# Optimization experiments

Measured on AMD Instinct MI355X. Metric: run time of the kernel, lower is better.

The kernel has to match this reference:

```python
import jax, jax.numpy as jnp
import numpy as np

N_NODES = 100000
N_EDGES = 1600000
NFEAT = 256
NHID = 64
NHEADS = 8
NCLASS = 97
ALPHA = 0.2  # leaky relu slope
EPS = 1e-16  # guard against isolated rows (pyGAT divides by e_rowsum directly)


def _sp_gat_layer(x, Wk, ak, src, dst, n_nodes, alpha, concat):
    """One SpGraphAttentionLayer (eval mode, dropout off).
    x: [N, f_in], Wk: [f_in, f_out], ak: [2*f_out].
    edge e_ij = exp(-leakyrelu(a . [h_i || h_j])), out[i] = sum_j e_ij h_j / sum_j e_ij.
    """
    h = x @ Wk                          # [N, f_out]
    f_out = Wk.shape[1]
    s_src = h @ ak[:f_out]              # [N] = a1 . h_i
    s_dst = h @ ak[f_out:]              # [N] = a2 . h_j
    e = jnp.exp(-jax.nn.leaky_relu(s_src[src] + s_dst[dst], negative_slope=alpha))  # [E]
    rowsum = jax.ops.segment_sum(e, src, num_segments=n_nodes)                       # [N]
    num = jax.ops.segment_sum(e[:, None] * h[dst], src, num_segments=n_nodes)        # [N, f_out]
    h_prime = num / (rowsum[:, None] + EPS)
    return jax.nn.elu(h_prime) if concat else h_prime


def setup_inputs() -> dict:
    key = jax.random.key(0)
    ks = jax.random.split(key, 6)
    gain = 1.414  # xavier gain used by pyGAT
    features = jax.random.normal(ks[0], (N_NODES, NFEAT), dtype=jnp.float32)
    edge_index = jax.random.randint(ks[1], (2, N_EDGES), 0, N_NODES, dtype=jnp.int64)
    W = jax.random.normal(ks[2], (NHEADS, NFEAT, NHID), dtype=jnp.float32) * (gain * np.sqrt(2.0 / (NFEAT + NHID)))
    a = jax.random.normal(ks[3], (NHEADS, 2 * NHID), dtype=jnp.float32) * (gain * np.sqrt(2.0 / (1 + 2 * NHID)))
    W_out = jax.random.normal(ks[4], (NHEADS * NHID, NCLASS), dtype=jnp.float32) * (gain * np.sqrt(2.0 / (NHEADS * NHID + NCLASS)))
    a_out = jax.random.normal(ks[5], (2 * NCLASS,), dtype=jnp.float32) * (gain * np.sqrt(2.0 / (1 + 2 * NCLASS)))
    return {"features": features, "W": W, "a": a, "W_out": W_out, "a_out": a_out, "edge_index": edge_index}


def reference(features, W, a, W_out, a_out, edge_index):
    src, dst = edge_index[0], edge_index[1]
    n = features.shape[0]
    # multi-head hidden layer, concat heads (loop over small fixed head count to bound memory)
    heads = [
        _sp_gat_layer(features, W[k], a[k], src, dst, n, ALPHA, concat=True)
        for k in range(W.shape[0])
    ]
    x = jnp.concatenate(heads, axis=1)  # [N, nheads*nhid]
    # output attention layer (concat=False), then elu + log_softmax as in SpGAT.forward
    x = _sp_gat_layer(x, W_out, a_out, src, dst, n, ALPHA, concat=False)
    return jax.nn.log_softmax(jax.nn.elu(x), axis=1)
```

## Files before the change

kernel.cpp:

```cpp
#include <hip/hip_runtime.h>
#include <hip/hip_bf16.h>
#include <stdint.h>

typedef __attribute__((ext_vector_type(8))) short short8;
typedef __attribute__((ext_vector_type(4))) float floatx4;
typedef uint32_t u32;

#define N_NODES 100000
#define N_EDGES 1600000
#define ALPHA_SLOPE 0.2f
#define EPS_F 1e-16f

static __device__ __forceinline__ float bf2f(ushort h) {
    u32 u = ((u32)h) << 16;
    return __builtin_bit_cast(float, u);
}
static __device__ __forceinline__ ushort f2bf(float f) {
    u32 u = __builtin_bit_cast(u32, f);
    u32 r = (u + 0x7fffu + ((u >> 16) & 1u)) >> 16;
    return (ushort)r;
}

__global__ __launch_bounds__(256) void conv_feat(
    const float* __restrict__ in, ushort* __restrict__ out, int n4)
{
    int i = blockIdx.x * 256 + threadIdx.x;
    if (i < n4) {
        float4 v = ((const float4*)in)[i];
        ushort4 o;
        o.x = f2bf(v.x); o.y = f2bf(v.y); o.z = f2bf(v.z); o.w = f2bf(v.w);
        ((ushort4*)out)[i] = o;
    }
}

__global__ __launch_bounds__(256) void pretranspose(
    const float* __restrict__ W, const float* __restrict__ Wout,
    const float* __restrict__ a, const float* __restrict__ aout,
    ushort* __restrict__ Bp1, ushort* __restrict__ Bp2,
    float* __restrict__ acol1, float* __restrict__ acol2)
{
    int idx = blockIdx.x * 256 + threadIdx.x;
    if (idx < 256 * 512) {
        int k = idx >> 9, n = idx & 511;
        int head = n >> 6, c = n & 63;
        Bp1[((size_t)(k >> 3) * 512 + n) * 8 + (k & 7)] = f2bf(W[head * 16384 + k * 64 + c]);
    }
    if (idx < 512 * 128) {
        int k = idx >> 7, n = idx & 127;
        ushort v = (n < 97) ? f2bf(Wout[k * 97 + n]) : (ushort)0;
        Bp2[((size_t)(k >> 3) * 128 + n) * 8 + (k & 7)] = v;
    }
    if (idx < 512) {
        int head = idx >> 6, c = idx & 63;
        acol1[idx * 2]     = a[head * 128 + c];
        acol1[idx * 2 + 1] = a[head * 128 + 64 + c];
    }
    if (idx < 128) {
        acol2[idx * 2]     = (idx < 97) ? aout[idx] : 0.f;
        acol2[idx * 2 + 1] = (idx < 97) ? aout[97 + idx] : 0.f;
    }
}

__global__ __launch_bounds__(256) void gemm_mfma(
    const ushort* __restrict__ A, const ushort* __restrict__ Bp,
    ushort* __restrict__ C, const float* __restrict__ acol,
    float* __restrict__ spair, int M, int K, int NP)
{
    __shared__ __align__(16) ushort Ald[4 * 128 * 8];
    const int tid = threadIdx.x;
    const int lane = tid & 63;
    const int wave = tid >> 6;
    const int wr = wave >> 1, wc = wave & 1;
    const int row0 = blockIdx.x * 128;
    const int col0 = blockIdx.y * 128;
    const int quad = lane >> 4;
    const int l16 = lane & 15;

    floatx4 acc[4][4] = {};

    for (int k0 = 0; k0 < K; k0 += 32) {
        __syncthreads();
#pragma unroll
        for (int i = 0; i < 2; ++i) {
            int q = i * 256 + tid;
            int r = q >> 2, kq = q & 3;
            int row = row0 + r;
            if (row >= M) row = M - 1;
            const uint4* src = (const uint4*)(A + (size_t)row * K + k0 + kq * 8);
            *(uint4*)(&Ald[((kq * 128 + r) * 8)]) = *src;
        }
        __syncthreads();

        short8 bfrag[4];
        int kqg = (k0 >> 3) + quad;
#pragma unroll
        for (int nt = 0; nt < 4; ++nt) {
            int col = col0 + wc * 64 + nt * 16 + l16;
            bfrag[nt] = *(const short8*)(Bp + ((size_t)kqg * NP + col) * 8);
        }
#pragma unroll
        for (int mt = 0; mt < 4; ++mt) {
            int r = wr * 64 + mt * 16 + l16;
            short8 afrag = *(const short8*)(&Ald[(quad * 128 + r) * 8]);
#pragma unroll
            for (int nt = 0; nt < 4; ++nt) {
                acc[mt][nt] = __builtin_amdgcn_mfma_f32_16x16x32_bf16(afrag, bfrag[nt], acc[mt][nt], 0, 0, 0);
            }
        }
    }

#pragma unroll
    for (int mt = 0; mt < 4; ++mt) {
#pragma unroll
        for (int rr = 0; rr < 4; ++rr) {
            int row = row0 + wr * 64 + mt * 16 + quad * 4 + rr;
            if (row < M) {
#pragma unroll
                for (int nt = 0; nt < 4; ++nt) {
                    int col = col0 + wc * 64 + nt * 16 + l16;
                    C[(size_t)row * NP + col] = f2bf(acc[mt][nt][rr]);
                }
            }
        }
    }

    float av1[4], av2[4];
#pragma unroll
    for (int nt = 0; nt < 4; ++nt) {
        int col = col0 + wc * 64 + nt * 16 + l16;
        av1[nt] = acol[col * 2];
        av2[nt] = acol[col * 2 + 1];
    }
    int g = (col0 + wc * 64) >> 6;
    int ng = NP >> 6;
#pragma unroll
    for (int mt = 0; mt < 4; ++mt) {
#pragma unroll
        for (int rr = 0; rr < 4; ++rr) {
            float p1 = 0.f, p2 = 0.f;
#pragma unroll
            for (int nt = 0; nt < 4; ++nt) {
                p1 = fmaf(acc[mt][nt][rr], av1[nt], p1);
                p2 = fmaf(acc[mt][nt][rr], av2[nt], p2);
            }
#pragma unroll
            for (int o = 1; o < 16; o <<= 1) {
                p1 += __shfl_xor(p1, o);
                p2 += __shfl_xor(p2, o);
            }
            int row = row0 + wr * 64 + mt * 16 + quad * 4 + rr;
            if (l16 == 0 && row < M) {
                atomicAdd(&spair[((size_t)row * ng + g) * 2], p1);
                atomicAdd(&spair[((size_t)row * ng + g) * 2 + 1], p2);
            }
        }
    }
}

__global__ __launch_bounds__(256) void hist(const int* __restrict__ ei, int* __restrict__ cnt, int E) {
    int e = blockIdx.x * 256 + threadIdx.x;
    if (e < E) atomicAdd(&cnt[ei[e]], 1);
}

__global__ __launch_bounds__(256) void scan_partial(const int* __restrict__ cnt, int* __restrict__ bsum, int N) {
    int idx = blockIdx.x * 256 + threadIdx.x;
    int v = (idx < N) ? cnt[idx] : 0;
#pragma unroll
    for (int o = 32; o; o >>= 1) v += __shfl_xor(v, o);
    __shared__ int ws[4];
    if ((threadIdx.x & 63) == 0) ws[threadIdx.x >> 6] = v;
    __syncthreads();
    if (threadIdx.x == 0) bsum[blockIdx.x] = ws[0] + ws[1] + ws[2] + ws[3];
}

__global__ __launch_bounds__(512) void scan_block(int* __restrict__ bsum, int nb) {
    __shared__ int s[512];
    int t = threadIdx.x;
    int v = (t < nb) ? bsum[t] : 0;
    s[t] = v;
    __syncthreads();
    for (int o = 1; o < 512; o <<= 1) {
        int u = (t >= o) ? s[t - o] : 0;
        __syncthreads();
        s[t] += u;
        __syncthreads();
    }
    if (t < nb) bsum[t] = s[t] - v;
}

__global__ __launch_bounds__(256) void scan_final(
    const int* __restrict__ cnt, const int* __restrict__ bsum,
    int* __restrict__ row_ptr, int N, int E)
{
    int b = blockIdx.x, t = threadIdx.x;
    int idx = b * 256 + t;
    int v = (idx < N) ? cnt[idx] : 0;
    __shared__ int s[256];
    s[t] = v;
    __syncthreads();
    for (int o = 1; o < 256; o <<= 1) {
        int u = (t >= o) ? s[t - o] : 0;
        __syncthreads();
        s[t] += u;
        __syncthreads();
    }
    if (idx < N) row_ptr[idx] = bsum[b] + s[t] - v;
    if (idx == 0) row_ptr[N] = E;
}

__global__ __launch_bounds__(256) void fill_csr(
    const int* __restrict__ ei, const int* __restrict__ row_ptr,
    int* __restrict__ cur, int* __restrict__ col_idx, int* __restrict__ srow,
    const float* __restrict__ spair1, float* __restrict__ ew1, int E)
{
    int e = blockIdx.x * 256 + threadIdx.x;
    if (e >= E) return;
    int s = ei[e];
    int d = ei[E + e];
    int p = atomicAdd(&cur[s], 1);
    int slot = row_ptr[s] + p;
    col_idx[slot] = d;
    srow[slot] = s;
    const float4* qs = (const float4*)(spair1 + (size_t)s * 16);
    const float4* qd = (const float4*)(spair1 + (size_t)d * 16);
    float ev[8];
#pragma unroll
    for (int h4 = 0; h4 < 4; ++h4) {
        float4 vs = qs[h4];
        float4 vd = qd[h4];
        float v0 = vs.x + vd.y;
        float v1 = vs.z + vd.w;
        float l0 = v0 > 0.f ? v0 : ALPHA_SLOPE * v0;
        float l1 = v1 > 0.f ? v1 : ALPHA_SLOPE * v1;
        ev[2 * h4] = __expf(-l0);
        ev[2 * h4 + 1] = __expf(-l1);
    }
    float4* dst = (float4*)(ew1 + (size_t)slot * 8);
    dst[0] = make_float4(ev[0], ev[1], ev[2], ev[3]);
    dst[1] = make_float4(ev[4], ev[5], ev[6], ev[7]);
}

__global__ __launch_bounds__(256) void ea1(
    const int* __restrict__ row_ptr, const int* __restrict__ col_idx,
    const ushort* __restrict__ h_all, const float* __restrict__ ew1,
    ushort* __restrict__ x1)
{
    int w = blockIdx.x * 4 + (threadIdx.x >> 6);
    int l = threadIdx.x & 63;
    int hl = l >> 3;
    int start = row_ptr[w], end = row_ptr[w + 1];
    float acc[8] = {};
    float re = 0.f;
    int j = start;
    for (; j + 4 <= end; j += 4) {
        int d0 = col_idx[j], d1 = col_idx[j + 1], d2 = col_idx[j + 2], d3 = col_idx[j + 3];
        float e0 = ew1[(size_t)j * 8 + hl];
        float e1 = ew1[(size_t)(j + 1) * 8 + hl];
        float e2 = ew1[(size_t)(j + 2) * 8 + hl];
        float e3 = ew1[(size_t)(j + 3) * 8 + hl];
        short8 v0 = *(const short8*)(h_all + (size_t)d0 * 512 + l * 8);
        short8 v1 = *(const short8*)(h_all + (size_t)d1 * 512 + l * 8);
        short8 v2 = *(const short8*)(h_all + (size_t)d2 * 512 + l * 8);
        short8 v3 = *(const short8*)(h_all + (size_t)d3 * 512 + l * 8);
        re += (e0 + e1) + (e2 + e3);
#pragma unroll
        for (int q = 0; q < 8; ++q) {
            float t0 = fmaf(e0, bf2f((ushort)v0[q]), e1 * bf2f((ushort)v1[q]));
            float t1 = fmaf(e2, bf2f((ushort)v2[q]), e3 * bf2f((ushort)v3[q]));
            acc[q] += t0 + t1;
        }
    }
    for (; j < end; ++j) {
        int d = col_idx[j];
        float e = ew1[(size_t)j * 8 + hl];
        short8 hv = *(const short8*)(h_all + (size_t)d * 512 + l * 8);
        re += e;
#pragma unroll
        for (int q = 0; q < 8; ++q)
            acc[q] = fmaf(e, bf2f((ushort)hv[q]), acc[q]);
    }
    float inv = 1.f / (re + EPS_F);
    short8 o;
#pragma unroll
    for (int q = 0; q < 8; ++q) {
        float p = acc[q] * inv;
        p = p > 0.f ? p : expm1f(p);
        o[q] = (short)f2bf(p);
    }
    *(short8*)(x1 + (size_t)w * 512 + l * 8) = o;
}

__global__ __launch_bounds__(256) void ew2k(
    const int* __restrict__ srow, const int* __restrict__ col_idx,
    const float* __restrict__ spair2, float* __restrict__ ew2, int E)
{
    int j = blockIdx.x * 256 + threadIdx.x;
    if (j < E) {
        float4 vs = *(const float4*)(spair2 + (size_t)srow[j] * 4);
        float4 vd = *(const float4*)(spair2 + (size_t)col_idx[j] * 4);
        float s = (vs.x + vs.z) + (vd.y + vd.w);
        float lr = s > 0.f ? s : ALPHA_SLOPE * s;
        ew2[j] = __expf(-lr);
    }
}

__global__ __launch_bounds__(256) void ea2(
    const int* __restrict__ row_ptr, const int* __restrict__ col_idx,
    const ushort* __restrict__ h2p, const float* __restrict__ ew2,
    float* __restrict__ out)
{
    int w = blockIdx.x * 4 + (threadIdx.x >> 6);
    int l = threadIdx.x & 63;
    int start = row_ptr[w], end = row_ptr[w + 1];
    float a0 = 0.f, a1 = 0.f, re = 0.f;
    int j = start;
    for (; j + 4 <= end; j += 4) {
        int d0 = col_idx[j], d1 = col_idx[j + 1], d2 = col_idx[j + 2], d3 = col_idx[j + 3];
        float e0 = ew2[j], e1 = ew2[j + 1], e2 = ew2[j + 2], e3 = ew2[j + 3];
        u32 h0 = *(const u32*)(h2p + (size_t)d0 * 128 + 2 * l);
        u32 h1 = *(const u32*)(h2p + (size_t)d1 * 128 + 2 * l);
        u32 h2 = *(const u32*)(h2p + (size_t)d2 * 128 + 2 * l);
        u32 h3 = *(const u32*)(h2p + (size_t)d3 * 128 + 2 * l);
        re += (e0 + e1) + (e2 + e3);
        a0 += fmaf(e0, bf2f((ushort)(h0 & 0xffffu)), e1 * bf2f((ushort)(h1 & 0xffffu)))
            + fmaf(e2, bf2f((ushort)(h2 & 0xffffu)), e3 * bf2f((ushort)(h3 & 0xffffu)));
        a1 += fmaf(e0, bf2f((ushort)(h0 >> 16)), e1 * bf2f((ushort)(h1 >> 16)))
            + fmaf(e2, bf2f((ushort)(h2 >> 16)), e3 * bf2f((ushort)(h3 >> 16)));
    }
    for (; j < end; ++j) {
        int d = col_idx[j];
        float e = ew2[j];
        u32 hv = *(const u32*)(h2p + (size_t)d * 128 + 2 * l);
        re += e;
        a0 = fmaf(e, bf2f((ushort)(hv & 0xffffu)), a0);
        a1 = fmaf(e, bf2f((ushort)(hv >> 16)), a1);
    }
    float inv = 1.f / (re + EPS_F);
    float v0 = a0 * inv, v1 = a1 * inv;
    v0 = v0 > 0.f ? v0 : expm1f(v0);
    v1 = v1 > 0.f ? v1 : expm1f(v1);
    int c0 = 2 * l, c1 = 2 * l + 1;
    bool val0 = c0 < 97, val1 = c1 < 97;
    float m = fmaxf(val0 ? v0 : -1e30f, val1 ? v1 : -1e30f);
#pragma unroll
    for (int o = 32; o; o >>= 1) m = fmaxf(m, __shfl_xor(m, o));
    float ex = (val0 ? __expf(v0 - m) : 0.f) + (val1 ? __expf(v1 - m) : 0.f);
#pragma unroll
    for (int o = 32; o; o >>= 1) ex += __shfl_xor(ex, o);
    float lt = m + logf(ex);
    if (val0) out[(size_t)w * 97 + c0] = v0 - lt;
    if (val1) out[(size_t)w * 97 + c1] = v1 - lt;
}

extern "C" void kernel_launch(void* const* d_in, const int* in_sizes, int n_in,
                              void* d_out, int out_size, void* d_ws, size_t ws_size,
                              hipStream_t stream)
{
    const float* feat = (const float*)d_in[0];
    const float* W    = (const float*)d_in[1];
    const float* a    = (const float*)d_in[2];
    const float* Wout = (const float*)d_in[3];
    const float* aout = (const float*)d_in[4];
    const int*   ei   = (const int*)d_in[5];
    float* out = (float*)d_out;

    const int N = N_NODES, E = N_EDGES;
    const int NB = (N + 255) / 256;

    char* base = (char*)d_ws;
    ushort* h_all = (ushort*)(base);
    ushort* x1    = (ushort*)(base + 102400000);
    ushort* featb = (ushort*)(base + 204800000);
    float*  ew1   = (float*)(base + 204800000);
    ushort* h2p   = (ushort*)(base + 204800000);
    char* tail = base + 256000000;
    float* spair1  = (float*)(tail + 0);
    float* spair2  = (float*)(tail + 6400000);
    int*   row_ptr = (int*)(tail + 8000000);
    int*   cnt     = (int*)(tail + 8400128);
    int*   col_idx = (int*)(tail + 8800128);
    int*   bsum    = (int*)(tail + 15200128);
    ushort* Bp1    = (ushort*)(tail + 15201920);
    ushort* Bp2    = (ushort*)(tail + 15464064);
    float* acol1   = (float*)(tail + 15595136);
    float* acol2   = (float*)(tail + 15599232);
    int*   srow    = (int*)(tail + 15600256);
    float* ew2     = (float*)(tail + 22000256);

    hipMemsetAsync(cnt, 0, (size_t)N * 4, stream);
    hipMemsetAsync(spair1, 0, (size_t)N * 16 * 4, stream);
    hipMemsetAsync(spair2, 0, (size_t)N * 4 * 4, stream);
    conv_feat<<<(N * 256 / 4 + 255) / 256, 256, 0, stream>>>(feat, featb, N * 256 / 4);
    pretranspose<<<512, 256, 0, stream>>>(W, Wout, a, aout, Bp1, Bp2, acol1, acol2);

    gemm_mfma<<<dim3(782, 4), 256, 0, stream>>>(featb, Bp1, h_all, acol1, spair1, N, 256, 512);

    hist<<<(E + 255) / 256, 256, 0, stream>>>(ei, cnt, E);
    scan_partial<<<NB, 256, 0, stream>>>(cnt, bsum, N);
    scan_block<<<1, 512, 0, stream>>>(bsum, NB);
    scan_final<<<NB, 256, 0, stream>>>(cnt, bsum, row_ptr, N, E);
    hipMemsetAsync(cnt, 0, (size_t)N * 4, stream);
    fill_csr<<<(E + 255) / 256, 256, 0, stream>>>(ei, row_ptr, cnt, col_idx, srow, spair1, ew1, E);

    ea1<<<N / 4, 256, 0, stream>>>(row_ptr, col_idx, h_all, ew1, x1);

    gemm_mfma<<<dim3(782, 1), 256, 0, stream>>>(x1, Bp2, h2p, acol2, spair2, N, 512, 128);
    ew2k<<<(E + 255) / 256, 256, 0, stream>>>(srow, col_idx, spair2, ew2, E);
    ea2<<<N / 4, 256, 0, stream>>>(row_ptr, col_idx, h2p, ew2, out);
}
```

Baseline: 920.7 us.

## Compute edge attention weights inline in aggregation kernels instead of materializing

Removes the precomputed per-edge weight arrays (ew1 with 8 floats per edge, ew2) and the ew2k kernel. The aggregation kernels now recompute exp(-leakyrelu(s_src+s_dst)) from per-node score arrays, split into separate src and dst arrays so each lane can gather its head's value. This cuts global memory writes and reads of edge weights and one launch, at the cost of extra scattered gathers of sdst per neighbour and redundant exp work across lanes. Output stores of x1 and the final logits also become nontemporal.

```diff
diff --git a/kernel.cpp b/kernel.cpp
--- a/kernel.cpp
+++ b/kernel.cpp
@@ -19,6 +19,10 @@
     u32 u = __builtin_bit_cast(u32, f);
     u32 r = (u + 0x7fffu + ((u >> 16) & 1u)) >> 16;
     return (ushort)r;
+}
+static __device__ __forceinline__ float edge_e(float s) {
+    float lr = s > 0.f ? s : ALPHA_SLOPE * s;
+    return __expf(-lr);
 }
 
 __global__ __launch_bounds__(256) void conv_feat(
@@ -64,7 +68,8 @@
 __global__ __launch_bounds__(256) void gemm_mfma(
     const ushort* __restrict__ A, const ushort* __restrict__ Bp,
     ushort* __restrict__ C, const float* __restrict__ acol,
-    float* __restrict__ spair, int M, int K, int NP)
+    float* __restrict__ ssrc_arr, float* __restrict__ sdst_arr,
+    int sstride, int M, int K, int NP)
 {
     __shared__ __align__(16) ushort Ald[4 * 128 * 8];
     const int tid = threadIdx.x;
@@ -132,7 +137,7 @@
         av2[nt] = acol[col * 2 + 1];
     }
     int g = (col0 + wc * 64) >> 6;
-    int ng = NP >> 6;
+    int goff = (sstride > 1) ? g : 0;
 #pragma unroll
     for (int mt = 0; mt < 4; ++mt) {
 #pragma unroll
@@ -150,8 +155,8 @@
             }
             int row = row0 + wr * 64 + mt * 16 + quad * 4 + rr;
             if (l16 == 0 && row < M) {
-                atomicAdd(&spair[((size_t)row * ng + g) * 2], p1);
-                atomicAdd(&spair[((size_t)row * ng + g) * 2 + 1], p2);
+                atomicAdd(&ssrc_arr[(size_t)row * sstride + goff], p1);
+                atomicAdd(&sdst_arr[(size_t)row * sstride + goff], p2);
             }
         }
     }
@@ -210,8 +215,7 @@
 
 __global__ __launch_bounds__(256) void fill_csr(
     const int* __restrict__ ei, const int* __restrict__ row_ptr,
-    int* __restrict__ cur, int* __restrict__ col_idx, int* __restrict__ srow,
-    const float* __restrict__ spair1, float* __restrict__ ew1, int E)
+    int* __restrict__ cur, int* __restrict__ col_idx, int* __restrict__ srow, int E)
 {
     int e = blockIdx.x * 256 + threadIdx.x;
     if (e >= E) return;
@@ -221,43 +225,27 @@
     int slot = row_ptr[s] + p;
     col_idx[slot] = d;
     srow[slot] = s;
-    const float4* qs = (const float4*)(spair1 + (size_t)s * 16);
-    const float4* qd = (const float4*)(spair1 + (size_t)d * 16);
-    float ev[8];
-#pragma unroll
-    for (int h4 = 0; h4 < 4; ++h4) {
-        float4 vs = qs[h4];
-        float4 vd = qd[h4];
-        float v0 = vs.x + vd.y;
-        float v1 = vs.z + vd.w;
-        float l0 = v0 > 0.f ? v0 : ALPHA_SLOPE * v0;
-        float l1 = v1 > 0.f ? v1 : ALPHA_SLOPE * v1;
-        ev[2 * h4] = __expf(-l0);
-        ev[2 * h4 + 1] = __expf(-l1);
-    }
-    float4* dst = (float4*)(ew1 + (size_t)slot * 8);
-    dst[0] = make_float4(ev[0], ev[1], ev[2], ev[3]);
-    dst[1] = make_float4(ev[4], ev[5], ev[6], ev[7]);
 }
 
 __global__ __launch_bounds__(256) void ea1(
     const int* __restrict__ row_ptr, const int* __restrict__ col_idx,
-    const ushort* __restrict__ h_all, const float* __restrict__ ew1,
-    ushort* __restrict__ x1)
+    const ushort* __restrict__ h_all, const float* __restrict__ ssrc1,
+    const float* __restrict__ sdst1, ushort* __restrict__ x1)
 {
     int w = blockIdx.x * 4 + (threadIdx.x >> 6);
     int l = threadIdx.x & 63;
     int hl = l >> 3;
     int start = row_ptr[w], end = row_ptr[w + 1];
+    float si = ssrc1[(size_t)w * 8 + hl];
     float acc[8] = {};
     float re = 0.f;
     int j = start;
     for (; j + 4 <= end; j += 4) {
         int d0 = col_idx[j], d1 = col_idx[j + 1], d2 = col_idx[j + 2], d3 = col_idx[j + 3];
-        float e0 = ew1[(size_t)j * 8 + hl];
-        float e1 = ew1[(size_t)(j + 1) * 8 + hl];
-        float e2 = ew1[(size_t)(j + 2) * 8 + hl];
-        float e3 = ew1[(size_t)(j + 3) * 8 + hl];
+        float e0 = edge_e(si + sdst1[(size_t)d0 * 8 + hl]);
+        float e1 = edge_e(si + sdst1[(size_t)d1 * 8 + hl]);
+        float e2 = edge_e(si + sdst1[(size_t)d2 * 8 + hl]);
+        float e3 = edge_e(si + sdst1[(size_t)d3 * 8 + hl]);
         short8 v0 = *(const short8*)(h_all + (size_t)d0 * 512 + l * 8);
         short8 v1 = *(const short8*)(h_all + (size_t)d1 * 512 + l * 8);
         short8 v2 = *(const short8*)(h_all + (size_t)d2 * 512 + l * 8);
@@ -272,7 +260,7 @@
     }
     for (; j < end; ++j) {
         int d = col_idx[j];
-        float e = ew1[(size_t)j * 8 + hl];
+        float e = edge_e(si + sdst1[(size_t)d * 8 + hl]);
         short8 hv = *(const short8*)(h_all + (size_t)d * 512 + l * 8);
         re += e;
 #pragma unroll
@@ -287,36 +275,26 @@
         p = p > 0.f ? p : expm1f(p);
         o[q] = (short)f2bf(p);
     }
-    *(short8*)(x1 + (size_t)w * 512 + l * 8) = o;
-}
-
-__global__ __launch_bounds__(256) void ew2k(
-    const int* __restrict__ srow, const int* __restrict__ col_idx,
-    const float* __restrict__ spair2, float* __restrict__ ew2, int E)
-{
-    int j = blockIdx.x * 256 + threadIdx.x;
-    if (j < E) {
-        float4 vs = *(const float4*)(spair2 + (size_t)srow[j] * 4);
-        float4 vd = *(const float4*)(spair2 + (size_t)col_idx[j] * 4);
-        float s = (vs.x + vs.z) + (vd.y + vd.w);
-        float lr = s > 0.f ? s : ALPHA_SLOPE * s;
-        ew2[j] = __expf(-lr);
-    }
+    __builtin_nontemporal_store(o, (short8*)(x1 + (size_t)w * 512 + l * 8));
 }
 
 __global__ __launch_bounds__(256) void ea2(
     const int* __restrict__ row_ptr, const int* __restrict__ col_idx,
-    const ushort* __restrict__ h2p, const float* __restrict__ ew2,
-    float* __restrict__ out)
+    const ushort* __restrict__ h2p, const float* __restrict__ s2src,
+    const float* __restrict__ s2dst, float* __restrict__ out)
 {
     int w = blockIdx.x * 4 + (threadIdx.x >> 6);
     int l = threadIdx.x & 63;
     int start = row_ptr[w], end = row_ptr[w + 1];
+    float si = s2src[w];
     float a0 = 0.f, a1 = 0.f, re = 0.f;
     int j = start;
     for (; j + 4 <= end; j += 4) {
         int d0 = col_idx[j], d1 = col_idx[j + 1], d2 = col_idx[j + 2], d3 = col_idx[j + 3];
-        float e0 = ew2[j], e1 = ew2[j + 1], e2 = ew2[j + 2], e3 = ew2[j + 3];
+        float e0 = edge_e(si + s2dst[d0]);
+        float e1 = edge_e(si + s2dst[d1]);
+        float e2 = edge_e(si + s2dst[d2]);
+        float e3 = edge_e(si + s2dst[d3]);
         u32 h0 = *(const u32*)(h2p + (size_t)d0 * 128 + 2 * l);
         u32 h1 = *(const u32*)(h2p + (size_t)d1 * 128 + 2 * l);
         u32 h2 = *(const u32*)(h2p + (size_t)d2 * 128 + 2 * l);
@@ -329,7 +307,7 @@
     }
     for (; j < end; ++j) {
         int d = col_idx[j];
-        float e = ew2[j];
+        float e = edge_e(si + s2dst[d]);
         u32 hv = *(const u32*)(h2p + (size_t)d * 128 + 2 * l);
         re += e;
         a0 = fmaf(e, bf2f((ushort)(hv & 0xffffu)), a0);
@@ -348,8 +326,8 @@
 #pragma unroll
     for (int o = 32; o; o >>= 1) ex += __shfl_xor(ex, o);
     float lt = m + logf(ex);
-    if (val0) out[(size_t)w * 97 + c0] = v0 - lt;
-    if (val1) out[(size_t)w * 97 + c1] = v1 - lt;
+    if (val0) __builtin_nontemporal_store(v0 - lt, out + (size_t)w * 97 + c0);
+    if (val1) __builtin_nontemporal_store(v1 - lt, out + (size_t)w * 97 + c1);
 }
 
 extern "C" void kernel_launch(void* const* d_in, const int* in_sizes, int n_in,
@@ -371,40 +349,38 @@
     ushort* h_all = (ushort*)(base);
     ushort* x1    = (ushort*)(base + 102400000);
     ushort* featb = (ushort*)(base + 204800000);
-    float*  ew1   = (float*)(base + 204800000);
     ushort* h2p   = (ushort*)(base + 204800000);
     char* tail = base + 256000000;
-    float* spair1  = (float*)(tail + 0);
-    float* spair2  = (float*)(tail + 6400000);
-    int*   row_ptr = (int*)(tail + 8000000);
-    int*   cnt     = (int*)(tail + 8400128);
-    int*   col_idx = (int*)(tail + 8800128);
-    int*   bsum    = (int*)(tail + 15200128);
-    ushort* Bp1    = (ushort*)(tail + 15201920);
-    ushort* Bp2    = (ushort*)(tail + 15464064);
-    float* acol1   = (float*)(tail + 15595136);
-    float* acol2   = (float*)(tail + 15599232);
-    int*   srow    = (int*)(tail + 15600256);
-    float* ew2     = (float*)(tail + 22000256);
+    float* ssrc1   = (float*)(tail + 0);
+    float* sdst1   = (float*)(tail + 3200000);
+    float* s2src   = (float*)(tail + 6400000);
+    float* s2dst   = (float*)(tail + 6800000);
+    int*   row_ptr = (int*)(tail + 7200000);
+    int*   cnt     = (int*)(tail + 7600128);
+    int*   col_idx = (int*)(tail + 8000128);
+    int*   bsum    = (int*)(tail + 14400128);
+    ushort* Bp1    = (ushort*)(tail + 14401920);
+    ushort* Bp2    = (ushort*)(tail + 14664064);
+    float* acol1   = (float*)(tail + 14795136);
+    float* acol2   = (float*)(tail + 14799232);
+    int*   srow    = (int*)(tail + 14800256);
 
     hipMemsetAsync(cnt, 0, (size_t)N * 4, stream);
-    hipMemsetAsync(spair1, 0, (size_t)N * 16 * 4, stream);
-    hipMemsetAsync(spair2, 0, (size_t)N * 4 * 4, stream);
+    hipMemsetAsync(ssrc1, 0, (size_t)7200000, stream);
     conv_feat<<<(N * 256 / 4 + 255) / 256, 256, 0, stream>>>(feat, featb, N * 256 / 4);
     pretranspose<<<512, 256, 0, stream>>>(W, Wout, a, aout, Bp1, Bp2, acol1, acol2);
 
-    gemm_mfma<<<dim3(782, 4), 256, 0, stream>>>(featb, Bp1, h_all, acol1, spair1, N, 256, 512);
+    gemm_mfma<<<dim3(782, 4), 256, 0, stream>>>(featb, Bp1, h_all, acol1, ssrc1, sdst1, 8, N, 256, 512);
 
     hist<<<(E + 255) / 256, 256, 0, stream>>>(ei, cnt, E);
     scan_partial<<<NB, 256, 0, stream>>>(cnt, bsum, N);
     scan_block<<<1, 512, 0, stream>>>(bsum, NB);
     scan_final<<<NB, 256, 0, stream>>>(cnt, bsum, row_ptr, N, E);
     hipMemsetAsync(cnt, 0, (size_t)N * 4, stream);
-    fill_csr<<<(E + 255) / 256, 256, 0, stream>>>(ei, row_ptr, cnt, col_idx, srow, spair1, ew1, E);
-
-    ea1<<<N / 4, 256, 0, stream>>>(row_ptr, col_idx, h_all, ew1, x1);
-
-    gemm_mfma<<<dim3(782, 1), 256, 0, stream>>>(x1, Bp2, h2p, acol2, spair2, N, 512, 128);
-    ew2k<<<(E + 255) / 256, 256, 0, stream>>>(srow, col_idx, spair2, ew2, E);
-    ea2<<<N / 4, 256, 0, stream>>>(row_ptr, col_idx, h2p, ew2, out);
-}
+    fill_csr<<<(E + 255) / 256, 256, 0, stream>>>(ei, row_ptr, cnt, col_idx, srow, E);
+
+    ea1<<<N / 4, 256, 0, stream>>>(row_ptr, col_idx, h_all, ssrc1, sdst1, x1);
+
+    gemm_mfma<<<dim3(782, 1), 256, 0, stream>>>(x1, Bp2, h2p, acol2, s2src, s2dst, 1, N, 512, 128);
+    ea2<<<N / 4, 256, 0, stream>>>(row_ptr, col_idx, h2p, s2src, s2dst, out);
+}
```

Result: faster. 865.5 us (-6.0%).
